# Performance work log

Hardware: AMD Instinct MI355X
Metric: run time of the kernel (lower is better)

Reference implementation:

```python
import jax, jax.numpy as jnp
import numpy as np

B, N, M = 8192, 64, 32          # batch, num_fields, embedding_dim
D = N * (N - 1) // 2            # 2016 pairwise-interaction rows of theta
OUT = 1024                      # block_out_dim
BN_EPS = 1e-5


def setup_inputs() -> dict:
    key = jax.random.key(0)
    k0, k1, k2, k3 = jax.random.split(key, 4)
    inputs = jax.random.normal(k0, (B, N * M), dtype=jnp.float32)
    W_z = jax.random.normal(k1, (N, N, M), dtype=jnp.float32) * 0.05
    theta = jax.random.normal(k2, (D, N), dtype=jnp.float32) * 0.05
    w_affine = jax.random.normal(k3, (OUT, N + D), dtype=jnp.float32) * 0.02
    b_affine = jnp.zeros((OUT,), dtype=jnp.float32)
    gamma = jnp.ones((OUT,), dtype=jnp.float32)
    beta = jnp.zeros((OUT,), dtype=jnp.float32)
    return {"inputs": inputs, "W_z": W_z, "theta": theta,
            "w_affine": w_affine, "b_affine": b_affine,
            "gamma": gamma, "beta": beta}


def reference(inputs, W_z, theta, w_affine, b_affine, gamma, beta):
    b = inputs.shape[0]
    x = inputs.reshape(b, N, M)                      # [B, N, M]
    # lz term: full quadratic form with W_z
    lz = jnp.einsum('bnm,dnm->bd', x, W_z)           # [B, N]
    # lp term: algebraically identical to einsum('bdnm,bdnm->bd') over
    # delta = einsum('bnm,dn->bdnm'): lp[b,d] = sum_n theta[d,n]^2 * sum_m x[b,n,m]^2
    x_sq = jnp.sum(x * x, axis=-1)                   # [B, N]
    lp = x_sq @ (theta * theta).T                    # [B, D]
    out = jnp.concatenate([lz, lp], axis=1)          # [B, N+D]
    out = out @ w_affine.T + b_affine                # [B, OUT]
    # BatchNorm1d in training mode (batch statistics, biased variance)
    mean = jnp.mean(out, axis=0)
    var = jnp.var(out, axis=0)
    out = (out - mean) * jax.lax.rsqrt(var + BN_EPS) * gamma + beta
    return out
```

## Files before the change

### kernel.cpp

```cpp
#include <hip/hip_runtime.h>
#include <stdint.h>

#define NROWS 8192
#define KX    2048
#define KA    2112
#define NF    64
#define DD    2016
#define WCOLS 2080
#define ODIM  1024
#define BN_EPS 1e-5f

#define A1_OT 32
#define A2_DC 8
#define A2_DPC 252
#define A2_OT 16

#define CONV_RPB 4
#define CONV_NB  (NROWS / CONV_RPB)
#define RED_NB   (ODIM * NF / 256)

#define A1A2_A1N 256
#define A1A2_A2E 768
#define A1A2_TOT 776

#define GBM 256
#define GBN 128
#define GBK 64
#define NT (KA / GBK)

using f32x4  = __attribute__((ext_vector_type(4))) float;
using bf16x8 = __attribute__((ext_vector_type(8))) short;

__device__ __forceinline__ short f2bf(float x) {
    uint32_t u = __float_as_uint(x);
    uint32_t r = (u + 0x7FFFu + ((u >> 16) & 1u)) >> 16;
    return (short)r;
}

__device__ __forceinline__ void gload16(const void* g, void* l) {
    __builtin_amdgcn_global_load_lds(
        (const __attribute__((address_space(1))) uint32_t*)g,
        (__attribute__((address_space(3))) uint32_t*)l, 16, 0, 0);
}

#define MFMA_BF16 __builtin_amdgcn_mfma_f32_16x16x32_bf16

__global__ __launch_bounds__(256) void conv_kern(const float* __restrict__ X,
                                                 short* __restrict__ Xa,
                                                 const float* __restrict__ partials,
                                                 short* __restrict__ Aw) {
    const int t = threadIdx.x;
    const int b = blockIdx.x;
    if (b < CONV_NB) {
#pragma unroll
        for (int r = 0; r < CONV_RPB; ++r) {
            const int row = b * CONV_RPB + r;
            const float4* xr = reinterpret_cast<const float4*>(X + (size_t)row * KX);
            float4 v0 = xr[t * 2];
            float4 v1 = xr[t * 2 + 1];
            bf16x8 s;
            s[0] = f2bf(v0.x); s[1] = f2bf(v0.y); s[2] = f2bf(v0.z); s[3] = f2bf(v0.w);
            s[4] = f2bf(v1.x); s[5] = f2bf(v1.y); s[6] = f2bf(v1.z); s[7] = f2bf(v1.w);
            short* outr = Xa + (size_t)row * KA;
            reinterpret_cast<bf16x8*>(outr)[t] = s;
            float sq = v0.x*v0.x + v0.y*v0.y + v0.z*v0.z + v0.w*v0.w
                     + v1.x*v1.x + v1.y*v1.y + v1.z*v1.z + v1.w*v1.w;
            sq += __shfl_xor(sq, 1);
            sq += __shfl_xor(sq, 2);
            if ((t & 3) == 0) outr[KX + (t >> 2)] = f2bf(sq - 32.0f);
        }
    } else {
        const int idx = (b - CONV_NB) * 256 + t;
        const int o = idx >> 6, n = idx & 63;
        float s = 0.f;
#pragma unroll
        for (int c = 0; c < A2_DC; ++c)
            s += partials[((size_t)c * ODIM + o) * NF + n];
        Aw[(size_t)o * KA + KX + n] = f2bf(s);
    }
}

__global__ __launch_bounds__(256) void a1a2_kern(short* __restrict__ Aw,
                                                 const float* __restrict__ Wa,
                                                 const float* __restrict__ Wz,
                                                 const float* __restrict__ theta,
                                                 float* __restrict__ partials,
                                                 float* __restrict__ sums) {
    const int bid = blockIdx.x;
    const int t = threadIdx.x;
    __shared__ __align__(16) float smem[4096];

    if (bid >= A1A2_A2E) {
        sums[(bid - A1A2_A2E) * 256 + t] = 0.f;
        return;
    }
    if (bid < A1A2_A1N) {
        const int k = (bid & 7) * 256 + t;
        const int o0 = (bid >> 3) * A1_OT;
        for (int idx = t; idx < A1_OT * 64; idx += 256)
            smem[idx] = Wa[(size_t)(o0 + (idx >> 6)) * WCOLS + (idx & 63)];
        float wz[64];
#pragma unroll
        for (int d = 0; d < 64; ++d) wz[d] = Wz[(size_t)d * KX + k];
        __syncthreads();
#pragma unroll 2
        for (int j = 0; j < A1_OT; ++j) {
            const float* war = &smem[j * 64];
            float acc = 0.f;
#pragma unroll
            for (int d = 0; d < 64; ++d) acc += war[d] * wz[d];
            Aw[(size_t)(o0 + j) * KA + k] = f2bf(acc);
        }
    } else {
        const int b = bid - A1A2_A1N;
        const int n = t & 63;
        const int g = t >> 6;
        const int chunk = b & 7;
        const int o0 = (b >> 3) * A2_OT;
        const int d0 = chunk * A2_DPC;
        float* waT = smem;
        for (int idx = t; idx < A2_OT * A2_DPC; idx += 256) {
            const int j = idx / A2_DPC, dd = idx - j * A2_DPC;
            waT[idx] = Wa[(size_t)(o0 + j) * WCOLS + NF + d0 + dd];
        }
        __syncthreads();
        float acc[A2_OT];
#pragma unroll
        for (int j = 0; j < A2_OT; ++j) acc[j] = 0.f;
        for (int i = g; i < A2_DPC; i += 4) {
            float th = theta[(size_t)(d0 + i) * NF + n];
            float th2 = th * th;
#pragma unroll
            for (int j = 0; j < A2_OT; ++j)
                acc[j] += waT[j * A2_DPC + i] * th2;
        }
        __syncthreads();
        float* red = smem;
#pragma unroll
        for (int j = 0; j < A2_OT; ++j) red[(g * A2_OT + j) * 64 + n] = acc[j];
        __syncthreads();
#pragma unroll
        for (int k2 = 0; k2 < A2_OT * 64 / 256; ++k2) {
            const int idx = t + k2 * 256;
            const int ol = idx >> 6, nn = idx & 63;
            float s = red[(0 * A2_OT + ol) * 64 + nn] + red[(1 * A2_OT + ol) * 64 + nn]
                    + red[(2 * A2_OT + ol) * 64 + nn] + red[(3 * A2_OT + ol) * 64 + nn];
            partials[((size_t)chunk * ODIM + o0 + ol) * NF + nn] = s;
        }
    }
}

__global__ __launch_bounds__(512) void gemm_kern(const short* __restrict__ Xa,
                                                 const short* __restrict__ Aw,
                                                 float* __restrict__ C,
                                                 float* __restrict__ sums) {
    __shared__ __align__(16) short As[3][GBM * GBK];
    __shared__ __align__(16) short Bs[3][GBN * GBK];
    const int tid  = threadIdx.x;
    const int lane = tid & 63;
    const int cl   = lane & 15;
    const int kq   = lane >> 4;
    const int wid  = tid >> 6;
    const int wr   = wid >> 1;
    const int wc   = wid & 1;
    const int bm = blockIdx.x * GBM;
    const int bn = blockIdx.y * GBN;

    f32x4 acc[4][4] = {};

    const short* gAs[4]; int ldA[4];
#pragma unroll
    for (int i = 0; i < 4; ++i) {
        const int c = tid + i * 512;
        const int row = c >> 3, cp = c & 7;
        gAs[i] = Xa + (size_t)(bm + row) * KA + (cp ^ (row & 7)) * 8;
        ldA[i] = c * 8;
    }
    const short* gBs[2]; int ldB[2];
#pragma unroll
    for (int i = 0; i < 2; ++i) {
        const int c = tid + i * 512;
        const int row = c >> 3, cp = c & 7;
        gBs[i] = Aw + (size_t)(bn + row) * KA + (cp ^ (row & 7)) * 8;
        ldB[i] = c * 8;
    }

    int offA[4][2], offB[4][2];
#pragma unroll
    for (int m = 0; m < 4; ++m) {
        const int r = wr * 64 + m * 16 + cl;
        offA[m][0] = r * GBK + ((kq)     ^ (r & 7)) * 8;
        offA[m][1] = r * GBK + ((4 + kq) ^ (r & 7)) * 8;
    }
#pragma unroll
    for (int n = 0; n < 4; ++n) {
        const int r = wc * 64 + n * 16 + cl;
        offB[n][0] = r * GBK + ((kq)     ^ (r & 7)) * 8;
        offB[n][1] = r * GBK + ((4 + kq) ^ (r & 7)) * 8;
    }

#define STAGE(buf, kt) do {                               \
        const int ko_ = (kt) * GBK;                       \
        gload16(gAs[0] + ko_, &As[buf][ldA[0]]);          \
        gload16(gAs[1] + ko_, &As[buf][ldA[1]]);          \
        gload16(gAs[2] + ko_, &As[buf][ldA[2]]);          \
        gload16(gAs[3] + ko_, &As[buf][ldA[3]]);          \
        gload16(gBs[0] + ko_, &Bs[buf][ldB[0]]);          \
        gload16(gBs[1] + ko_, &Bs[buf][ldB[1]]);          \
    } while (0)

#define TILE(cbuf, sbuf, kt) do {                                            \
        if ((kt) + 2 < NT) STAGE(sbuf, (kt) + 2);                            \
        bf16x8 a_[4][2], b_[4][2];                                           \
        _Pragma("unroll")                                                    \
        for (int m = 0; m < 4; ++m) {                                        \
            a_[m][0] = *reinterpret_cast<const bf16x8*>(&As[cbuf][offA[m][0]]); \
            a_[m][1] = *reinterpret_cast<const bf16x8*>(&As[cbuf][offA[m][1]]); \
        }                                                                    \
        _Pragma("unroll")                                                    \
        for (int n = 0; n < 4; ++n) {                                        \
            b_[n][0] = *reinterpret_cast<const bf16x8*>(&Bs[cbuf][offB[n][0]]); \
            b_[n][1] = *reinterpret_cast<const bf16x8*>(&Bs[cbuf][offB[n][1]]); \
        }                                                                    \
        asm volatile("s_waitcnt lgkmcnt(0)" ::: "memory");                   \
        __builtin_amdgcn_sched_barrier(0);                                   \
        __builtin_amdgcn_s_setprio(1);                                       \
        _Pragma("unroll")                                                    \
        for (int m = 0; m < 4; ++m)                                          \
            _Pragma("unroll")                                                \
            for (int n = 0; n < 4; ++n) {                                    \
                acc[m][n] = MFMA_BF16(a_[m][0], b_[n][0], acc[m][n], 0, 0, 0); \
                acc[m][n] = MFMA_BF16(a_[m][1], b_[n][1], acc[m][n], 0, 0, 0); \
            }                                                                \
        __builtin_amdgcn_s_setprio(0);                                       \
        if ((kt) + 2 < NT)                                                   \
            asm volatile("s_waitcnt vmcnt(6)" ::: "memory");                 \
        else if ((kt) + 1 < NT)                                              \
            asm volatile("s_waitcnt vmcnt(0)" ::: "memory");                 \
        __builtin_amdgcn_s_barrier();                                        \
    } while (0)

    STAGE(0, 0);
    STAGE(1, 1);
    asm volatile("s_waitcnt vmcnt(6)" ::: "memory");
    __builtin_amdgcn_s_barrier();

    for (int kt = 0; kt < NT; kt += 3) {
        TILE(0, 2, kt);
        TILE(1, 0, kt + 1);
        TILE(2, 1, kt + 2);
    }
#undef TILE
#undef STAGE

    const int rlo = kq * 4;
#pragma unroll
    for (int n = 0; n < 4; ++n) {
        const int col = bn + wc * 64 + n * 16 + cl;
        float s = 0.f, q = 0.f;
#pragma unroll
        for (int m = 0; m < 4; ++m) {
            const int rowb = bm + wr * 64 + m * 16 + rlo;
#pragma unroll
            for (int r2 = 0; r2 < 4; ++r2) {
                float v = acc[m][n][r2];
                C[(size_t)(rowb + r2) * ODIM + col] = v;
                s += v; q += v * v;
            }
        }
        s += __shfl_xor(s, 16); s += __shfl_xor(s, 32);
        q += __shfl_xor(q, 16); q += __shfl_xor(q, 32);
        if (lane < 16) {
            atomicAdd(&sums[col], s);
            atomicAdd(&sums[ODIM + col], q);
        }
    }
}

__global__ __launch_bounds__(256) void bn_apply(float* __restrict__ C,
                                                const float* __restrict__ sums,
                                                const float* __restrict__ gamma,
                                                const float* __restrict__ beta) {
    const int g = blockIdx.x * 256 + threadIdx.x;
    const int c4 = g & (ODIM / 4 - 1);
    const int row0 = g >> 8;
    const float inv = 1.0f / (float)NROWS;
    float4 sc, sh;
    {
        float4 s0 = reinterpret_cast<const float4*>(sums)[c4];
        float4 q0 = reinterpret_cast<const float4*>(sums + ODIM)[c4];
        float4 gm = reinterpret_cast<const float4*>(gamma)[c4];
        float4 bt = reinterpret_cast<const float4*>(beta)[c4];
        float m, v;
        m = s0.x * inv; v = q0.x * inv - m * m; sc.x = gm.x * rsqrtf(v + BN_EPS); sh.x = bt.x - m * sc.x;
        m = s0.y * inv; v = q0.y * inv - m * m; sc.y = gm.y * rsqrtf(v + BN_EPS); sh.y = bt.y - m * sc.y;
        m = s0.z * inv; v = q0.z * inv - m * m; sc.z = gm.z * rsqrtf(v + BN_EPS); sh.z = bt.z - m * sc.z;
        m = s0.w * inv; v = q0.w * inv - m * m; sc.w = gm.w * rsqrtf(v + BN_EPS); sh.w = bt.w - m * sc.w;
    }
#pragma unroll
    for (int r = 0; r < 4; ++r) {
        const size_t i = (size_t)(row0 + r * 2048) * (ODIM / 4) + c4;
        float4 v = reinterpret_cast<const float4*>(C)[i];
        v.x = v.x * sc.x + sh.x;
        v.y = v.y * sc.y + sh.y;
        v.z = v.z * sc.z + sh.z;
        v.w = v.w * sc.w + sh.w;
        reinterpret_cast<float4*>(C)[i] = v;
    }
}

extern "C" void kernel_launch(void* const* d_in, const int* in_sizes, int n_in,
                              void* d_out, int out_size, void* d_ws, size_t ws_size,
                              hipStream_t stream) {
    const float* X     = (const float*)d_in[0];
    const float* Wz    = (const float*)d_in[1];
    const float* theta = (const float*)d_in[2];
    const float* Wa    = (const float*)d_in[3];
    const float* gamma = (const float*)d_in[5];
    const float* beta  = (const float*)d_in[6];
    float* out = (float*)d_out;

    char* ws = (char*)d_ws;
    float* sums = (float*)ws;
    short* Xa = (short*)(ws + 16384);
    short* Aw = (short*)(ws + 16384 + (size_t)NROWS * KA * 2);
    float* partials = (float*)(ws + 16384 + (size_t)NROWS * KA * 2
                                        + (size_t)ODIM * KA * 2);

    a1a2_kern<<<A1A2_TOT, 256, 0, stream>>>(Aw, Wa, Wz, theta, partials, sums);
    conv_kern<<<CONV_NB + RED_NB, 256, 0, stream>>>(X, Xa, partials, Aw);
    gemm_kern<<<dim3(NROWS / GBM, ODIM / GBN), 512, 0, stream>>>(Xa, Aw, out, sums);
    bn_apply<<<NROWS / 4 * ODIM / 4 / 256, 256, 0, stream>>>(out, sums, gamma, beta);
}
```

Baseline: 100.9 us.

## Fuse BatchNorm apply into GEMM epilogue via cooperative grid sync

Result: slower. 129.3 us (+28.1%).

```diff
diff --git a/kernel.cpp b/kernel.cpp
--- a/kernel.cpp
+++ b/kernel.cpp
@@ -1,4 +1,5 @@
 #include <hip/hip_runtime.h>
+#include <hip/hip_cooperative_groups.h>
 #include <stdint.h>
 
 #define NROWS 8192
@@ -150,10 +151,12 @@
     }
 }
 
-__global__ __launch_bounds__(512) void gemm_kern(const short* __restrict__ Xa,
-                                                 const short* __restrict__ Aw,
-                                                 float* __restrict__ C,
-                                                 float* __restrict__ sums) {
+__global__ __launch_bounds__(512) void gemm_bn(const short* __restrict__ Xa,
+                                               const short* __restrict__ Aw,
+                                               float* __restrict__ C,
+                                               float* __restrict__ sums,
+                                               const float* __restrict__ gamma,
+                                               const float* __restrict__ beta) {
     __shared__ __align__(16) short As[3][GBM * GBK];
     __shared__ __align__(16) short Bs[3][GBN * GBK];
     const int tid  = threadIdx.x;
@@ -259,15 +262,12 @@
         const int col = bn + wc * 64 + n * 16 + cl;
         float s = 0.f, q = 0.f;
 #pragma unroll
-        for (int m = 0; m < 4; ++m) {
-            const int rowb = bm + wr * 64 + m * 16 + rlo;
+        for (int m = 0; m < 4; ++m)
 #pragma unroll
             for (int r2 = 0; r2 < 4; ++r2) {
                 float v = acc[m][n][r2];
-                C[(size_t)(rowb + r2) * ODIM + col] = v;
                 s += v; q += v * v;
             }
-        }
         s += __shfl_xor(s, 16); s += __shfl_xor(s, 32);
         q += __shfl_xor(q, 16); q += __shfl_xor(q, 32);
         if (lane < 16) {
@@ -275,37 +275,24 @@
             atomicAdd(&sums[ODIM + col], q);
         }
     }
-}
-
-__global__ __launch_bounds__(256) void bn_apply(float* __restrict__ C,
-                                                const float* __restrict__ sums,
-                                                const float* __restrict__ gamma,
-                                                const float* __restrict__ beta) {
-    const int g = blockIdx.x * 256 + threadIdx.x;
-    const int c4 = g & (ODIM / 4 - 1);
-    const int row0 = g >> 8;
+
+    cooperative_groups::this_grid().sync();
+
     const float inv = 1.0f / (float)NROWS;
-    float4 sc, sh;
-    {
-        float4 s0 = reinterpret_cast<const float4*>(sums)[c4];
-        float4 q0 = reinterpret_cast<const float4*>(sums + ODIM)[c4];
-        float4 gm = reinterpret_cast<const float4*>(gamma)[c4];
-        float4 bt = reinterpret_cast<const float4*>(beta)[c4];
-        float m, v;
-        m = s0.x * inv; v = q0.x * inv - m * m; sc.x = gm.x * rsqrtf(v + BN_EPS); sh.x = bt.x - m * sc.x;
-        m = s0.y * inv; v = q0.y * inv - m * m; sc.y = gm.y * rsqrtf(v + BN_EPS); sh.y = bt.y - m * sc.y;
-        m = s0.z * inv; v = q0.z * inv - m * m; sc.z = gm.z * rsqrtf(v + BN_EPS); sh.z = bt.z - m * sc.z;
-        m = s0.w * inv; v = q0.w * inv - m * m; sc.w = gm.w * rsqrtf(v + BN_EPS); sh.w = bt.w - m * sc.w;
-    }
-#pragma unroll
-    for (int r = 0; r < 4; ++r) {
-        const size_t i = (size_t)(row0 + r * 2048) * (ODIM / 4) + c4;
-        float4 v = reinterpret_cast<const float4*>(C)[i];
-        v.x = v.x * sc.x + sh.x;
-        v.y = v.y * sc.y + sh.y;
-        v.z = v.z * sc.z + sh.z;
-        v.w = v.w * sc.w + sh.w;
-        reinterpret_cast<float4*>(C)[i] = v;
+#pragma unroll
+    for (int n = 0; n < 4; ++n) {
+        const int col = bn + wc * 64 + n * 16 + cl;
+        const float mean = sums[col] * inv;
+        const float var  = sums[ODIM + col] * inv - mean * mean;
+        const float sc   = gamma[col] * rsqrtf(var + BN_EPS);
+        const float sh   = beta[col] - mean * sc;
+#pragma unroll
+        for (int m = 0; m < 4; ++m) {
+            const int rowb = bm + wr * 64 + m * 16 + rlo;
+#pragma unroll
+            for (int r2 = 0; r2 < 4; ++r2)
+                C[(size_t)(rowb + r2) * ODIM + col] = acc[m][n][r2] * sc + sh;
+        }
     }
 }
 
@@ -329,6 +316,12 @@
 
     a1a2_kern<<<A1A2_TOT, 256, 0, stream>>>(Aw, Wa, Wz, theta, partials, sums);
     conv_kern<<<CONV_NB + RED_NB, 256, 0, stream>>>(X, Xa, partials, Aw);
-    gemm_kern<<<dim3(NROWS / GBM, ODIM / GBN), 512, 0, stream>>>(Xa, Aw, out, sums);
-    bn_apply<<<NROWS / 4 * ODIM / 4 / 256, 256, 0, stream>>>(out, sums, gamma, beta);
-}
+
+    const short* Xa_c = Xa;
+    const short* Aw_c = Aw;
+    void* args[] = {(void*)&Xa_c, (void*)&Aw_c, (void*)&out, (void*)&sums,
+                    (void*)&gamma, (void*)&beta};
+    hipLaunchCooperativeKernel((const void*)gemm_bn,
+                               dim3(NROWS / GBM, ODIM / GBN), dim3(512),
+                               args, 0, stream);
+}
```

## Use 4-wave GEMM blocks with 128x64 warp tiles and K-step 32

Applied to the files above, without the earlier changes.

After: 158.8 us. 57.3% more time.

```diff
diff --git a/kernel.cpp b/kernel.cpp
--- a/kernel.cpp
+++ b/kernel.cpp
@@ -25,8 +25,7 @@
 
 #define GBM 256
 #define GBN 128
-#define GBK 64
-#define NT (KA / GBK)
+#define NT (KA / 32)
 
 using f32x4  = __attribute__((ext_vector_type(4))) float;
 using bf16x8 = __attribute__((ext_vector_type(8))) short;
@@ -150,57 +149,55 @@
     }
 }
 
-__global__ __launch_bounds__(512) void gemm_kern(const short* __restrict__ Xa,
-                                                 const short* __restrict__ Aw,
-                                                 float* __restrict__ C,
-                                                 float* __restrict__ sums) {
-    __shared__ __align__(16) short As[3][GBM * GBK];
-    __shared__ __align__(16) short Bs[3][GBN * GBK];
+__global__ __launch_bounds__(256, 2) void gemm_kern(const short* __restrict__ Xa,
+                                                    const short* __restrict__ Aw,
+                                                    float* __restrict__ C,
+                                                    float* __restrict__ sums) {
+    __shared__ __align__(16) short As[3][GBM * 32];
+    __shared__ __align__(16) short Bs[3][GBN * 32];
     const int tid  = threadIdx.x;
     const int lane = tid & 63;
     const int cl   = lane & 15;
-    const int kq   = lane >> 4;
+    const int lq   = lane >> 4;
     const int wid  = tid >> 6;
     const int wr   = wid >> 1;
     const int wc   = wid & 1;
     const int bm = blockIdx.x * GBM;
     const int bn = blockIdx.y * GBN;
 
-    f32x4 acc[4][4] = {};
+    f32x4 acc[8][4] = {};
 
     const short* gAs[4]; int ldA[4];
 #pragma unroll
     for (int i = 0; i < 4; ++i) {
-        const int c = tid + i * 512;
-        const int row = c >> 3, cp = c & 7;
-        gAs[i] = Xa + (size_t)(bm + row) * KA + (cp ^ (row & 7)) * 8;
+        const int c = tid + i * 256;
+        const int r = c >> 2, q = (c & 3) ^ ((r >> 1) & 3);
+        gAs[i] = Xa + (size_t)(bm + r) * KA + q * 8;
         ldA[i] = c * 8;
     }
     const short* gBs[2]; int ldB[2];
 #pragma unroll
     for (int i = 0; i < 2; ++i) {
-        const int c = tid + i * 512;
-        const int row = c >> 3, cp = c & 7;
-        gBs[i] = Aw + (size_t)(bn + row) * KA + (cp ^ (row & 7)) * 8;
+        const int c = tid + i * 256;
+        const int r = c >> 2, q = (c & 3) ^ ((r >> 1) & 3);
+        gBs[i] = Aw + (size_t)(bn + r) * KA + q * 8;
         ldB[i] = c * 8;
     }
 
-    int offA[4][2], offB[4][2];
-#pragma unroll
-    for (int m = 0; m < 4; ++m) {
-        const int r = wr * 64 + m * 16 + cl;
-        offA[m][0] = r * GBK + ((kq)     ^ (r & 7)) * 8;
-        offA[m][1] = r * GBK + ((4 + kq) ^ (r & 7)) * 8;
+    int offA[8], offB[4];
+#pragma unroll
+    for (int m = 0; m < 8; ++m) {
+        const int r = wr * 128 + m * 16 + cl;
+        offA[m] = r * 32 + (lq ^ ((r >> 1) & 3)) * 8;
     }
 #pragma unroll
     for (int n = 0; n < 4; ++n) {
         const int r = wc * 64 + n * 16 + cl;
-        offB[n][0] = r * GBK + ((kq)     ^ (r & 7)) * 8;
-        offB[n][1] = r * GBK + ((4 + kq) ^ (r & 7)) * 8;
+        offB[n] = r * 32 + (lq ^ ((r >> 1) & 3)) * 8;
     }
 
 #define STAGE(buf, kt) do {                               \
-        const int ko_ = (kt) * GBK;                       \
+        const int ko_ = (kt) * 32;                        \
         gload16(gAs[0] + ko_, &As[buf][ldA[0]]);          \
         gload16(gAs[1] + ko_, &As[buf][ldA[1]]);          \
         gload16(gAs[2] + ko_, &As[buf][ldA[2]]);          \
@@ -211,27 +208,21 @@
 
 #define TILE(cbuf, sbuf, kt) do {                                            \
         if ((kt) + 2 < NT) STAGE(sbuf, (kt) + 2);                            \
-        bf16x8 a_[4][2], b_[4][2];                                           \
+        bf16x8 a_[8], b_[4];                                                 \
         _Pragma("unroll")                                                    \
-        for (int m = 0; m < 4; ++m) {                                        \
-            a_[m][0] = *reinterpret_cast<const bf16x8*>(&As[cbuf][offA[m][0]]); \
-            a_[m][1] = *reinterpret_cast<const bf16x8*>(&As[cbuf][offA[m][1]]); \
-        }                                                                    \
+        for (int m = 0; m < 8; ++m)                                          \
+            a_[m] = *reinterpret_cast<const bf16x8*>(&As[cbuf][offA[m]]);    \
         _Pragma("unroll")                                                    \
-        for (int n = 0; n < 4; ++n) {                                        \
-            b_[n][0] = *reinterpret_cast<const bf16x8*>(&Bs[cbuf][offB[n][0]]); \
-            b_[n][1] = *reinterpret_cast<const bf16x8*>(&Bs[cbuf][offB[n][1]]); \
-        }                                                                    \
+        for (int n = 0; n < 4; ++n)                                          \
+            b_[n] = *reinterpret_cast<const bf16x8*>(&Bs[cbuf][offB[n]]);    \
         asm volatile("s_waitcnt lgkmcnt(0)" ::: "memory");                   \
         __builtin_amdgcn_sched_barrier(0);                                   \
         __builtin_amdgcn_s_setprio(1);                                       \
         _Pragma("unroll")                                                    \
-        for (int m = 0; m < 4; ++m)                                          \
+        for (int m = 0; m < 8; ++m)                                          \
             _Pragma("unroll")                                                \
-            for (int n = 0; n < 4; ++n) {                                    \
-                acc[m][n] = MFMA_BF16(a_[m][0], b_[n][0], acc[m][n], 0, 0, 0); \
-                acc[m][n] = MFMA_BF16(a_[m][1], b_[n][1], acc[m][n], 0, 0, 0); \
-            }                                                                \
+            for (int n = 0; n < 4; ++n)                                      \
+                acc[m][n] = MFMA_BF16(a_[m], b_[n], acc[m][n], 0, 0, 0);     \
         __builtin_amdgcn_s_setprio(0);                                       \
         if ((kt) + 2 < NT)                                                   \
             asm volatile("s_waitcnt vmcnt(6)" ::: "memory");                 \
@@ -253,14 +244,14 @@
 #undef TILE
 #undef STAGE
 
-    const int rlo = kq * 4;
+    const int rlo = lq * 4;
 #pragma unroll
     for (int n = 0; n < 4; ++n) {
         const int col = bn + wc * 64 + n * 16 + cl;
         float s = 0.f, q = 0.f;
 #pragma unroll
-        for (int m = 0; m < 4; ++m) {
-            const int rowb = bm + wr * 64 + m * 16 + rlo;
+        for (int m = 0; m < 8; ++m) {
+            const int rowb = bm + wr * 128 + m * 16 + rlo;
 #pragma unroll
             for (int r2 = 0; r2 < 4; ++r2) {
                 float v = acc[m][n][r2];
@@ -329,6 +320,6 @@
 
     a1a2_kern<<<A1A2_TOT, 256, 0, stream>>>(Aw, Wa, Wz, theta, partials, sums);
     conv_kern<<<CONV_NB + RED_NB, 256, 0, stream>>>(X, Xa, partials, Aw);
-    gemm_kern<<<dim3(NROWS / GBM, ODIM / GBN), 512, 0, stream>>>(Xa, Aw, out, sums);
+    gemm_kern<<<dim3(NROWS / GBM, ODIM / GBN), 256, 0, stream>>>(Xa, Aw, out, sums);
     bn_apply<<<NROWS / 4 * ODIM / 4 / 256, 256, 0, stream>>>(out, sums, gamma, beta);
 }
```
